# Kernel tuning notes

Measured on AMD Instinct MI355X. Metric: run time of the kernel, lower is better.

Reference implementation:

```python
import jax, jax.numpy as jnp
import numpy as np

D = 4096  # input_dim
H = 4096  # hidden_dim


def setup_inputs() -> dict:
    key = jax.random.key(0)
    k_x, k_w, k_b, k_v, k_c = jax.random.split(key, 5)
    x = jax.random.uniform(k_x, (D, 1), dtype=jnp.float32)  # observed pixel values
    w = jax.random.normal(k_w, (H, D), dtype=jnp.float32) * 0.02
    b = jax.random.normal(k_b, (D, 1), dtype=jnp.float32) * 0.02
    v = jax.random.normal(k_v, (D, H), dtype=jnp.float32) * 0.02
    c = jax.random.normal(k_c, (H, 1), dtype=jnp.float32) * 0.02
    return {"x": x, "w": w, "b": b, "v": v, "c": c}


def reference(x, w, b, v, c):
    # Original loop: a_0 = c; a_{i+1} = a_i + w[:, i] * x[i]
    # => a_i = c + sum_{j < i} w[:, j] * x[j]  (exclusive cumsum of rank-1 updates)
    wx = w * x[:, 0][None, :]                      # [H, D]
    cum = jnp.cumsum(wx, axis=1)                   # inclusive cumsum over columns
    A = c + jnp.pad(cum[:, :-1], ((0, 0), (1, 0)))  # exclusive cumsum -> a_i in column i, [H, D]
    h = jax.nn.sigmoid(A)                          # h_i = sigmoid(a_i), [H, D]
    # p_i = sigmoid(v[i, :] @ h_i + b[i])
    logits = jnp.einsum("ih,hi->i", v, h)[:, None] + b  # [D, 1]
    p_x = jax.nn.sigmoid(logits)                   # [D, 1]
    return p_x
```

## Files before the change

### kernel.cpp

```cpp
#include <hip/hip_runtime.h>

#define D_DIM 4096
#define H_DIM 4096
#define HB 16
#define IB 256
#define SP 260
#define NBLK (H_DIM / HB)
#define NT (D_DIM / IB)

__device__ __forceinline__ float fast_sigmoid(float a) {
    return __builtin_amdgcn_rcpf(1.0f + __expf(-a));
}

template <bool ATOMIC>
__global__ __launch_bounds__(1024, 1) void nade_main_kernel(
    const float* __restrict__ x,
    const float* __restrict__ w,
    const float* __restrict__ v,
    const float* __restrict__ c,
    float* __restrict__ part)
{
    __shared__ float S[2][HB][SP];
    __shared__ float partial[D_DIM];
    __shared__ float xs[D_DIM];

    const int tid  = threadIdx.x;
    const int wv   = tid >> 6;
    const int lane = tid & 63;
    const int q    = tid & 3;
    const int il   = tid >> 2;
    const int h0   = blockIdx.x * HB;

    for (int i = tid; i < D_DIM; i += 1024) {
        xs[i] = x[i];
        partial[i] = 0.0f;
    }
    const int h = h0 + wv;
    const float* wrow = w + (size_t)h * D_DIM;
    float carry = c[h];
    __syncthreads();

    auto scan_tile = [&](int t, int buf) {
        const int i0 = t * IB;
        float4 wp = *reinterpret_cast<const float4*>(wrow + i0 + 4 * lane);
        float4 xp = *reinterpret_cast<const float4*>(&xs[i0 + 4 * lane]);
        float p0 = wp.x * xp.x, p1 = wp.y * xp.y, p2 = wp.z * xp.z, p3 = wp.w * xp.w;
        float sum4 = p0 + p1 + p2 + p3;
        float incl = sum4;
        #pragma unroll
        for (int off = 1; off < 64; off <<= 1) {
            float tv = __shfl_up(incl, off, 64);
            incl += (lane >= off) ? tv : 0.0f;
        }
        float e = carry + incl - sum4;
        float a0 = e;
        float a1 = a0 + p0;
        float a2 = a1 + p1;
        float a3 = a2 + p2;
        float4 sv;
        sv.x = fast_sigmoid(a0);
        sv.y = fast_sigmoid(a1);
        sv.z = fast_sigmoid(a2);
        sv.w = fast_sigmoid(a3);
        *reinterpret_cast<float4*>(&S[buf][wv][4 * lane]) = sv;
        carry += __shfl(incl, 63, 64);
    };

    scan_tile(0, 0);

    for (int t = 0; t < NT; ++t) {
        __syncthreads();
        if (t + 1 < NT) scan_tile(t + 1, (t + 1) & 1);
        const int i = t * IB + il;
        float4 vp = *reinterpret_cast<const float4*>(v + (size_t)i * H_DIM + h0 + 4 * q);
        const float* Sb = &S[t & 1][0][0];
        float s0 = Sb[(4 * q + 0) * SP + il];
        float s1 = Sb[(4 * q + 1) * SP + il];
        float s2 = Sb[(4 * q + 2) * SP + il];
        float s3 = Sb[(4 * q + 3) * SP + il];
        float acc = vp.x * s0 + vp.y * s1 + vp.z * s2 + vp.w * s3;
        acc += __shfl_xor(acc, 1, 64);
        acc += __shfl_xor(acc, 2, 64);
        if (q == 0) partial[i] += acc;
    }
    __syncthreads();

    if (ATOMIC) {
        for (int i = tid; i < D_DIM; i += 1024)
            atomicAdd(&part[i], partial[i]);
    } else {
        for (int i = tid; i < D_DIM; i += 1024)
            part[(size_t)blockIdx.x * D_DIM + i] = partial[i];
    }
}

__global__ __launch_bounds__(1024, 1) void nade_reduce_kernel(
    const float* __restrict__ part,
    const float* __restrict__ b,
    float* __restrict__ out)
{
    __shared__ float red[16][64];
    const int tid = threadIdx.x;
    const int bg  = tid >> 6;
    const int il  = tid & 63;
    const int i   = blockIdx.x * 64 + il;
    float s = 0.0f;
    #pragma unroll
    for (int j = 0; j < NBLK / 16; ++j)
        s += part[(size_t)(bg * (NBLK / 16) + j) * D_DIM + i];
    red[bg][il] = s;
    __syncthreads();
    if (tid < 64) {
        float t = b[blockIdx.x * 64 + tid];
        #pragma unroll
        for (int j = 0; j < 16; ++j) t += red[j][tid];
        out[blockIdx.x * 64 + tid] = fast_sigmoid(t);
    }
}

__global__ __launch_bounds__(256, 1) void nade_final_atomic(
    const float* __restrict__ logits,
    const float* __restrict__ b,
    float* __restrict__ out)
{
    const int i = blockIdx.x * 256 + threadIdx.x;
    out[i] = fast_sigmoid(logits[i] + b[i]);
}

extern "C" void kernel_launch(void* const* d_in, const int* in_sizes, int n_in,
                              void* d_out, int out_size, void* d_ws, size_t ws_size,
                              hipStream_t stream)
{
    const float* x = (const float*)d_in[0];
    const float* w = (const float*)d_in[1];
    const float* b = (const float*)d_in[2];
    const float* v = (const float*)d_in[3];
    const float* c = (const float*)d_in[4];
    float* out = (float*)d_out;
    float* ws  = (float*)d_ws;

    const size_t need = (size_t)NBLK * D_DIM * sizeof(float);
    if (ws_size >= need) {
        nade_main_kernel<false><<<NBLK, 1024, 0, stream>>>(x, w, v, c, ws);
        nade_reduce_kernel<<<D_DIM / 64, 1024, 0, stream>>>(ws, b, out);
    } else {
        hipMemsetAsync(d_ws, 0, D_DIM * sizeof(float), stream);
        nade_main_kernel<true><<<NBLK, 1024, 0, stream>>>(x, w, v, c, ws);
        nade_final_atomic<<<D_DIM / 256, 256, 0, stream>>>(ws, b, out);
    }
}
```

Measured before the change: 44.76 us.

## Split scan across D via cooperative grid sync with fp16 LDS tiles

Replaces the per-row sequential scan over all of D with a 2D decomposition: each of 256 blocks handles a 128x512 (h,i) tile, computes local prefix sums, writes per-segment totals to workspace, then does a grid-wide cooperative sync to add cross-segment carries before the sigmoid and the v-dot. Intermediate pre-activations are stored in LDS as fp16 to fit the larger tile, and the partials reduction shrinks from 256 to 32 rows. This removes the long serial dependency along D and the large partial buffer, at the cost of a grid barrier, fp16 precision loss on the cumulative sums, and dropping the small-workspace fallback path.

```diff
diff --git a/kernel.cpp b/kernel.cpp
--- a/kernel.cpp
+++ b/kernel.cpp
@@ -1,130 +1,158 @@
 #include <hip/hip_runtime.h>
+#include <hip/hip_fp16.h>
+#include <hip/hip_cooperative_groups.h>
 
 #define D_DIM 4096
 #define H_DIM 4096
-#define HB 16
-#define IB 256
-#define SP 260
-#define NBLK (H_DIM / HB)
-#define NT (D_DIM / IB)
+#define HS 128
+#define IS 512
+#define NE (D_DIM / IS)
+#define NS (H_DIM / HS)
+#define SPAD 520
+
+namespace cg = cooperative_groups;
 
 __device__ __forceinline__ float fast_sigmoid(float a) {
     return __builtin_amdgcn_rcpf(1.0f + __expf(-a));
 }
 
-template <bool ATOMIC>
-__global__ __launch_bounds__(1024, 1) void nade_main_kernel(
+__global__ __launch_bounds__(1024, 1) void nade_coop_kernel(
     const float* __restrict__ x,
     const float* __restrict__ w,
     const float* __restrict__ v,
     const float* __restrict__ c,
+    float* __restrict__ Tws,
     float* __restrict__ part)
 {
-    __shared__ float S[2][HB][SP];
-    __shared__ float partial[D_DIM];
-    __shared__ float xs[D_DIM];
+    __shared__ __half S[HS][SPAD];
 
     const int tid  = threadIdx.x;
     const int wv   = tid >> 6;
     const int lane = tid & 63;
-    const int q    = tid & 3;
-    const int il   = tid >> 2;
-    const int h0   = blockIdx.x * HB;
+    const int s    = blockIdx.x >> 3;
+    const int e    = blockIdx.x & 7;
+    const int h0   = s * HS;
+    const int i0   = e * IS;
 
-    for (int i = tid; i < D_DIM; i += 1024) {
-        xs[i] = x[i];
-        partial[i] = 0.0f;
-    }
-    const int h = h0 + wv;
-    const float* wrow = w + (size_t)h * D_DIM;
-    float carry = c[h];
-    __syncthreads();
+    const float* xp = x + i0 + 8 * lane;
+    float4 x0 = *reinterpret_cast<const float4*>(xp);
+    float4 x1 = *reinterpret_cast<const float4*>(xp + 4);
 
-    auto scan_tile = [&](int t, int buf) {
-        const int i0 = t * IB;
-        float4 wp = *reinterpret_cast<const float4*>(wrow + i0 + 4 * lane);
-        float4 xp = *reinterpret_cast<const float4*>(&xs[i0 + 4 * lane]);
-        float p0 = wp.x * xp.x, p1 = wp.y * xp.y, p2 = wp.z * xp.z, p3 = wp.w * xp.w;
-        float sum4 = p0 + p1 + p2 + p3;
-        float incl = sum4;
+    const float* wbase = w + ((size_t)(h0 + wv * 8)) * D_DIM + i0 + 8 * lane;
+
+    float4 wc0 = *reinterpret_cast<const float4*>(wbase);
+    float4 wc1 = *reinterpret_cast<const float4*>(wbase + 4);
+
+    #pragma unroll
+    for (int k = 0; k < 8; ++k) {
+        float4 wn0, wn1;
+        if (k < 7) {
+            const float* p = wbase + (size_t)(k + 1) * D_DIM;
+            wn0 = *reinterpret_cast<const float4*>(p);
+            wn1 = *reinterpret_cast<const float4*>(p + 4);
+        }
+        float p0 = wc0.x * x0.x, p1 = wc0.y * x0.y, p2 = wc0.z * x0.z, p3 = wc0.w * x0.w;
+        float p4 = wc1.x * x1.x, p5 = wc1.y * x1.y, p6 = wc1.z * x1.z, p7 = wc1.w * x1.w;
+        float s8 = ((p0 + p1) + (p2 + p3)) + ((p4 + p5) + (p6 + p7));
+        float incl = s8;
         #pragma unroll
         for (int off = 1; off < 64; off <<= 1) {
             float tv = __shfl_up(incl, off, 64);
             incl += (lane >= off) ? tv : 0.0f;
         }
-        float e = carry + incl - sum4;
-        float a0 = e;
-        float a1 = a0 + p0;
-        float a2 = a1 + p1;
-        float a3 = a2 + p2;
-        float4 sv;
-        sv.x = fast_sigmoid(a0);
-        sv.y = fast_sigmoid(a1);
-        sv.z = fast_sigmoid(a2);
-        sv.w = fast_sigmoid(a3);
-        *reinterpret_cast<float4*>(&S[buf][wv][4 * lane]) = sv;
-        carry += __shfl(incl, 63, 64);
-    };
+        float a = incl - s8;
+        float l0 = a;       a += p0;
+        float l1 = a;       a += p1;
+        float l2 = a;       a += p2;
+        float l3 = a;       a += p3;
+        float l4 = a;       a += p4;
+        float l5 = a;       a += p5;
+        float l6 = a;       a += p6;
+        float l7 = a;
+        union { __half2 h2[4]; uint4 u; } P;
+        P.h2[0] = __floats2half2_rn(l0, l1);
+        P.h2[1] = __floats2half2_rn(l2, l3);
+        P.h2[2] = __floats2half2_rn(l4, l5);
+        P.h2[3] = __floats2half2_rn(l6, l7);
+        const int row = wv * 8 + k;
+        *reinterpret_cast<uint4*>(&S[row][8 * lane]) = P.u;
+        if (lane == 63) Tws[e * H_DIM + h0 + row] = incl;
+        wc0 = wn0; wc1 = wn1;
+    }
 
-    scan_tile(0, 0);
+    __threadfence();
+    cg::this_grid().sync();
 
-    for (int t = 0; t < NT; ++t) {
-        __syncthreads();
-        if (t + 1 < NT) scan_tile(t + 1, (t + 1) & 1);
-        const int i = t * IB + il;
-        float4 vp = *reinterpret_cast<const float4*>(v + (size_t)i * H_DIM + h0 + 4 * q);
-        const float* Sb = &S[t & 1][0][0];
-        float s0 = Sb[(4 * q + 0) * SP + il];
-        float s1 = Sb[(4 * q + 1) * SP + il];
-        float s2 = Sb[(4 * q + 2) * SP + il];
-        float s3 = Sb[(4 * q + 3) * SP + il];
-        float acc = vp.x * s0 + vp.y * s1 + vp.z * s2 + vp.w * s3;
-        acc += __shfl_xor(acc, 1, 64);
-        acc += __shfl_xor(acc, 2, 64);
-        if (q == 0) partial[i] += acc;
+    {
+        const int row = tid >> 3;
+        const int sub = tid & 7;
+        float base = c[h0 + row];
+        for (int ee = 0; ee < e; ++ee)
+            base += Tws[ee * H_DIM + h0 + row];
+        #pragma unroll
+        for (int k = 0; k < 8; ++k) {
+            const int m = sub + 8 * k;
+            uint4* p = reinterpret_cast<uint4*>(&S[row][m * 8]);
+            union { __half2 h2[4]; uint4 u; } P;
+            P.u = *p;
+            #pragma unroll
+            for (int j = 0; j < 4; ++j) {
+                float2 f = __half22float2(P.h2[j]);
+                f.x = fast_sigmoid(f.x + base);
+                f.y = fast_sigmoid(f.y + base);
+                P.h2[j] = __floats2half2_rn(f.x, f.y);
+            }
+            *p = P.u;
+        }
     }
     __syncthreads();
 
-    if (ATOMIC) {
-        for (int i = tid; i < D_DIM; i += 1024)
-            atomicAdd(&part[i], partial[i]);
-    } else {
-        for (int i = tid; i < D_DIM; i += 1024)
-            part[(size_t)blockIdx.x * D_DIM + i] = partial[i];
+    {
+        const int il   = tid >> 1;
+        const int half = tid & 1;
+        const int i    = i0 + il;
+        const float* vp = v + (size_t)i * H_DIM + h0 + half * 64;
+        float acc0 = 0.0f, acc1 = 0.0f;
+        #pragma unroll
+        for (int k = 0; k < 8; ++k) {
+            float4 va = *reinterpret_cast<const float4*>(vp + 8 * k);
+            float4 vb = *reinterpret_cast<const float4*>(vp + 8 * k + 4);
+            const int hh = half * 64 + 8 * k;
+            acc0 += va.x * __half2float(S[hh + 0][il])
+                  + va.y * __half2float(S[hh + 1][il])
+                  + va.z * __half2float(S[hh + 2][il])
+                  + va.w * __half2float(S[hh + 3][il]);
+            acc1 += vb.x * __half2float(S[hh + 4][il])
+                  + vb.y * __half2float(S[hh + 5][il])
+                  + vb.z * __half2float(S[hh + 6][il])
+                  + vb.w * __half2float(S[hh + 7][il]);
+        }
+        float acc = acc0 + acc1;
+        acc += __shfl_xor(acc, 1, 64);
+        if (half == 0) part[(size_t)s * D_DIM + i] = acc;
     }
 }
 
-__global__ __launch_bounds__(1024, 1) void nade_reduce_kernel(
+__global__ __launch_bounds__(1024, 1) void nade_out_kernel(
     const float* __restrict__ part,
     const float* __restrict__ b,
     float* __restrict__ out)
 {
-    __shared__ float red[16][64];
+    __shared__ float red[4][260];
     const int tid = threadIdx.x;
-    const int bg  = tid >> 6;
-    const int il  = tid & 63;
-    const int i   = blockIdx.x * 64 + il;
-    float s = 0.0f;
+    const int il  = tid & 255;
+    const int g   = tid >> 8;
+    const int i   = blockIdx.x * 256 + il;
+    float sacc = 0.0f;
     #pragma unroll
-    for (int j = 0; j < NBLK / 16; ++j)
-        s += part[(size_t)(bg * (NBLK / 16) + j) * D_DIM + i];
-    red[bg][il] = s;
+    for (int j = 0; j < 8; ++j)
+        sacc += part[(size_t)(g * 8 + j) * D_DIM + i];
+    red[g][il] = sacc;
     __syncthreads();
-    if (tid < 64) {
-        float t = b[blockIdx.x * 64 + tid];
-        #pragma unroll
-        for (int j = 0; j < 16; ++j) t += red[j][tid];
-        out[blockIdx.x * 64 + tid] = fast_sigmoid(t);
+    if (g == 0) {
+        float t = b[i] + red[0][il] + red[1][il] + red[2][il] + red[3][il];
+        out[i] = fast_sigmoid(t);
     }
-}
-
-__global__ __launch_bounds__(256, 1) void nade_final_atomic(
-    const float* __restrict__ logits,
-    const float* __restrict__ b,
-    float* __restrict__ out)
-{
-    const int i = blockIdx.x * 256 + threadIdx.x;
-    out[i] = fast_sigmoid(logits[i] + b[i]);
 }
 
 extern "C" void kernel_launch(void* const* d_in, const int* in_sizes, int n_in,
@@ -137,15 +165,13 @@
     const float* v = (const float*)d_in[3];
     const float* c = (const float*)d_in[4];
     float* out = (float*)d_out;
-    float* ws  = (float*)d_ws;
 
-    const size_t need = (size_t)NBLK * D_DIM * sizeof(float);
-    if (ws_size >= need) {
-        nade_main_kernel<false><<<NBLK, 1024, 0, stream>>>(x, w, v, c, ws);
-        nade_reduce_kernel<<<D_DIM / 64, 1024, 0, stream>>>(ws, b, out);
-    } else {
-        hipMemsetAsync(d_ws, 0, D_DIM * sizeof(float), stream);
-        nade_main_kernel<true><<<NBLK, 1024, 0, stream>>>(x, w, v, c, ws);
-        nade_final_atomic<<<D_DIM / 256, 256, 0, stream>>>(ws, b, out);
-    }
+    float* Tws  = (float*)d_ws;
+    float* part = Tws + (size_t)NE * H_DIM;
+
+    void* args[] = { (void*)&x, (void*)&w, (void*)&v, (void*)&c,
+                     (void*)&Tws, (void*)&part };
+    hipLaunchCooperativeKernel((const void*)nade_coop_kernel,
+                               dim3(NS * NE), dim3(1024), args, 0, stream);
+    nade_out_kernel<<<16, 1024, 0, stream>>>(part, b, out);
 }
```

Result: slower. 146.8 us (+228.0%).
